# Optimization experiments

Hardware: AMD Instinct MI355X
Metric: run time of the kernel (lower is better)

Reference implementation:

```python
import jax, jax.numpy as jnp
import numpy as np

C = 16          # n_channels
HIDDEN = 128
ALPHA_THRESH = 0.1
STEP_SIZE = 1.0


def _perception_kernel():
    ident = jnp.array([[0., 0., 0.], [0., 1., 0.], [0., 0., 0.]], dtype=jnp.float32)
    dx = jnp.array([[-0.125, 0., 0.125], [-0.25, 0., 0.25], [-0.125, 0., 0.125]], dtype=jnp.float32)
    dy = dx.T  # angle = 0 -> no rotation
    k = jnp.stack([ident, dx, dy])                 # [3,3,3]
    return jnp.tile(k, (C, 1, 1))[:, None]          # [3C,1,3,3], OIHW, groups=C


def _wrap_pad(x):
    # circular padding of 1 on H and W (torus)
    return jnp.pad(x, ((0, 0), (0, 0), (1, 1), (1, 1)), mode='wrap')


def _living_mask(x):
    alpha = x[:, 3:4]                               # [B,1,H,W]
    pooled = jax.lax.reduce_window(_wrap_pad(alpha), -jnp.inf, jax.lax.max,
                                   (1, 1, 3, 3), (1, 1, 1, 1), 'VALID')
    return pooled > ALPHA_THRESH                    # [B,1,H,W] bool


def _perceive(x):
    kern = _perception_kernel()
    return jax.lax.conv_general_dilated(
        _wrap_pad(x), kern, window_strides=(1, 1), padding='VALID',
        feature_group_count=C,
        dimension_numbers=('NCHW', 'OIHW', 'NCHW'))   # [B,3C,H,W]


def setup_inputs() -> dict:
    key = jax.random.key(0)
    k1, k2, k3, k4 = jax.random.split(key, 4)
    B, H, W = 32, 256, 256
    x = jax.random.uniform(k1, (B, C, H, W), dtype=jnp.float32)
    fire_mask = jax.random.randint(k2, (B, 1, H, W), 0, 2).astype(jnp.int32)
    # Conv2d(48->128,1) and Conv2d(128->16,1) weights, stored as matrices
    w1 = jax.random.normal(k3, (HIDDEN, 3 * C), dtype=jnp.float32) * (1.0 / np.sqrt(3 * C))
    b1 = jnp.zeros((HIDDEN,), dtype=jnp.float32)
    w2 = jax.random.normal(k4, (C, HIDDEN), dtype=jnp.float32) * (1.0 / np.sqrt(HIDDEN))
    b2 = jnp.zeros((C,), dtype=jnp.float32)
    return {"x": x, "w1": w1, "b1": b1, "w2": w2, "b2": b2, "fire_mask": fire_mask}


def reference(x, w1, b1, w2, b2, fire_mask):
    pre_life = _living_mask(x)                                   # [B,1,H,W]
    y = _perceive(x)                                             # [B,3C,H,W]
    h = jax.nn.relu(jnp.einsum('bchw,oc->bohw', y, w1) + b1[None, :, None, None])
    dx = (jnp.einsum('bchw,oc->bohw', h, w2) + b2[None, :, None, None]) * STEP_SIZE
    dx = dx * fire_mask.astype(dx.dtype)                          # stochastic update mask
    x_new = x + dx
    post_life = _living_mask(x_new)
    life = (pre_life & post_life).astype(x_new.dtype)
    return x_new * life
```

## Files before the change

kernel.cpp:

```cpp
#include <hip/hip_runtime.h>
#include <hip/hip_bf16.h>


#define CCH 16
#define HID 128
#define HH 256
#define WW 256
#define BB 32

typedef __attribute__((ext_vector_type(8))) short bf16x8;
typedef __attribute__((ext_vector_type(4))) float f32x4;
typedef __attribute__((ext_vector_type(4))) int i32x4;
typedef __attribute__((ext_vector_type(2))) unsigned int u32x2;

union bfpack {
  u32x2 w2[2];
  bf16x8 v;
};

__device__ inline unsigned short f2bf(float f) {
  unsigned int u = __float_as_uint(f);
  u += 0x7FFFu + ((u >> 16) & 1u);
  return (unsigned short)(u >> 16);
}
__device__ inline float bf2f(unsigned short s) {
  return __uint_as_float(((unsigned int)s) << 16);
}
__device__ inline unsigned int cvtpk2(float a, float b) {
  union { __hip_bfloat162 h; unsigned int u; } cv;
  cv.h = __float22bfloat162_rn(make_float2(a, b));
  return cv.u;
}

__global__ __launch_bounds__(256) void pack_weights_kernel(
    const float* __restrict__ w1, const float* __restrict__ w2,
    unsigned short* __restrict__ w1p, unsigned short* __restrict__ w2p) {
  const int tid = blockIdx.x * 256 + threadIdx.x;
  if (tid < 2048) {
    const int l = tid & 63, m = (tid >> 6) & 7, ks = (tid >> 9) & 1,
              pl = (tid >> 10) & 1;
    const int row = m * 16 + (l & 15);
    const int kb = ks * 32 + (l >> 4) * 8;
    const size_t off = ((((size_t)pl * 2 + ks) * 8 + m) * 64 + l) * 8;
#pragma unroll
    for (int j = 0; j < 8; ++j) {
      const int k = kb + j;
      const int cc = k >> 2, f = k & 3;
      const float v = (f < 3) ? w1[row * 48 + cc * 3 + f] : 0.0f;
      const unsigned short hi = f2bf(v);
      w1p[off + j] = (pl == 0) ? hi : f2bf(v - bf2f(hi));
    }
  } else if (tid < 2560) {
    const int t2 = tid - 2048;
    const int l = t2 & 63, ks = (t2 >> 6) & 3, pl = (t2 >> 8) & 1;
    const int row = l & 15;
    const int kb = ks * 32 + (l >> 4) * 8;
    const size_t off = (((size_t)pl * 4 + ks) * 64 + l) * 8;
#pragma unroll
    for (int j = 0; j < 8; ++j) {
      const float v = w2[row * 128 + kb + j];
      const unsigned short hi = f2bf(v);
      w2p[off + j] = (pl == 0) ? hi : f2bf(v - bf2f(hi));
    }
  }
}

__device__ inline int swkey(int row) {
  return (((row >> 2) ^ ((row & 3) << 2)) & 15) << 3;
}

__global__ __launch_bounds__(256, 4) void nca_mfma_kernel(
    const float* __restrict__ x, const float* __restrict__ b1,
    const float* __restrict__ b2, const unsigned short* __restrict__ w1p,
    const unsigned short* __restrict__ w2p, const int* __restrict__ fire,
    float* __restrict__ out, float* __restrict__ alpha_ws,
    unsigned char* __restrict__ pre_ws) {
  __shared__ __align__(16) unsigned char smem[24576];
  unsigned char* Ys = smem;
  unsigned char* Hsm = smem + 8192;

  const int L = blockIdx.x;
  const int orig = ((L & 7) << 12) | (L >> 3);
  const int b = orig >> 10;
  const int h = (orig >> 2) & 255;
  const int wt = orig & 3;
  const int tid = threadIdx.x;
  const int wv = tid >> 6, lane = tid & 63, g = lane >> 4, ln = lane & 15;
  const int c = wv * 4 + g;
  const int q = ln;
  const int gcol0 = wt * 64 + q * 4;
  const int hm = (h + 255) & 255, hp = (h + 1) & 255;

  const float* xc = x + (size_t)(b * CCH + c) * (HH * WW);
  const f32x4 t4 = *(const f32x4*)(xc + (size_t)hm * WW + gcol0);
  const f32x4 m4 = *(const f32x4*)(xc + (size_t)h * WW + gcol0);
  const f32x4 o4 = *(const f32x4*)(xc + (size_t)hp * WW + gcol0);
  f32x4 av, bv;
#pragma unroll
  for (int j = 0; j < 4; ++j) {
    av[j] = 0.125f * (t4[j] + o4[j]) + 0.25f * m4[j];
    bv[j] = 0.125f * (o4[j] - t4[j]);
  }

  float haA = 0.f, haB = 0.f, hcm = 0.f;
  if (q == 0 || q == 15) {
    const int gc = (q == 15) ? ((wt * 64 + 64) & 255) : ((wt * 64 + 255) & 255);
    const float t = xc[(size_t)hm * WW + gc];
    const float m = xc[(size_t)h * WW + gc];
    const float bo = xc[(size_t)hp * WW + gc];
    haA = 0.125f * (t + bo) + 0.25f * m;
    haB = 0.125f * (bo - t);
    hcm = fmaxf(fmaxf(t, m), bo);
  }

  {
    float aLs = __shfl(av[3], lane - 1, 64);
    float bLs = __shfl(bv[3], lane - 1, 64);
    float aRs = __shfl(av[0], lane + 1, 64);
    float bRs = __shfl(bv[0], lane + 1, 64);
    if (q == 0) { aLs = haA; bLs = haB; }
    if (q == 15) { aRs = haA; bRs = haB; }

    const int c8 = c * 8;
#pragma unroll
    for (int i = 0; i < 4; ++i) {
      const float aR = (i < 3) ? av[i + 1] : aRs;
      const float aL = (i > 0) ? av[i - 1] : aLs;
      const float bR = (i < 3) ? bv[i + 1] : bRs;
      const float bL = (i > 0) ? bv[i - 1] : bLs;
      const float y0 = m4[i];
      const float y1 = aR - aL;
      const float y2 = bL + 2.0f * bv[i] + bR;
      const int px = q * 4 + i;
      u32x2 w;
      w[0] = cvtpk2(y0, y1);
      w[1] = cvtpk2(y2, 0.0f);
      *(u32x2*)(Ys + px * 128 + (c8 ^ swkey(px))) = w;
    }

    if (c == 3) {
      f32x4 cm4;
#pragma unroll
      for (int j = 0; j < 4; ++j) cm4[j] = fmaxf(fmaxf(t4[j], m4[j]), o4[j]);
      float cmL = __shfl(cm4[3], lane - 1, 64);
      float cmR = __shfl(cm4[0], lane + 1, 64);
      if (q == 0) cmL = hcm;
      if (q == 15) cmR = hcm;
      const float p0 = fmaxf(fmaxf(cmL, cm4[0]), cm4[1]);
      const float p1 = fmaxf(fmaxf(cm4[0], cm4[1]), cm4[2]);
      const float p2 = fmaxf(fmaxf(cm4[1], cm4[2]), cm4[3]);
      const float p3 = fmaxf(fmaxf(cm4[2], cm4[3]), cmR);
      const unsigned int pb = (p0 > 0.1f ? 1u : 0u) |
                              ((p1 > 0.1f ? 1u : 0u) << 8) |
                              ((p2 > 0.1f ? 1u : 0u) << 16) |
                              ((p3 > 0.1f ? 1u : 0u) << 24);
      const size_t pix0 = ((size_t)b * HH + h) * WW + gcol0;
      *(unsigned int*)(pre_ws + pix0) = pb;
    }
  }

  bf16x8 A1[2][4];
#pragma unroll
  for (int mi = 0; mi < 2; ++mi)
#pragma unroll
    for (int f = 0; f < 4; ++f)
      A1[mi][f] = *(const bf16x8*)(
          w1p + (((size_t)f * 8 + (wv * 2 + mi)) * 64 + lane) * 8);
  f32x4 b1v[2];
#pragma unroll
  for (int mi = 0; mi < 2; ++mi)
    b1v[mi] = *(const f32x4*)(b1 + (wv * 2 + mi) * 16 + g * 4);

  __syncthreads();

#pragma unroll
  for (int ni = 0; ni < 4; ++ni) {
    const int pxb = ni * 16 + ln;
    const int sk = swkey(pxb);
    const unsigned char* rb = Ys + pxb * 128;
    bfpack B0, B1;
    B0.w2[0] = *(const u32x2*)(rb + ((g * 16) ^ sk));
    B0.w2[1] = *(const u32x2*)(rb + ((g * 16 + 8) ^ sk));
    B1.w2[0] = *(const u32x2*)(rb + ((64 + g * 16) ^ sk));
    B1.w2[1] = *(const u32x2*)(rb + ((64 + g * 16 + 8) ^ sk));
#pragma unroll
    for (int mi = 0; mi < 2; ++mi) {
      f32x4 a = (f32x4){0.f, 0.f, 0.f, 0.f};
      a = __builtin_amdgcn_mfma_f32_16x16x32_bf16(A1[mi][0], B0.v, a, 0, 0, 0);
      a = __builtin_amdgcn_mfma_f32_16x16x32_bf16(A1[mi][1], B1.v, a, 0, 0, 0);
      a = __builtin_amdgcn_mfma_f32_16x16x32_bf16(A1[mi][2], B0.v, a, 0, 0, 0);
      a = __builtin_amdgcn_mfma_f32_16x16x32_bf16(A1[mi][3], B1.v, a, 0, 0, 0);
      const int hid0 = (wv * 2 + mi) * 16 + g * 4;
      u32x2 hv;
      hv[0] = cvtpk2(fmaxf(a[0] + b1v[mi][0], 0.f),
                     fmaxf(a[1] + b1v[mi][1], 0.f));
      hv[1] = cvtpk2(fmaxf(a[2] + b1v[mi][2], 0.f),
                     fmaxf(a[3] + b1v[mi][3], 0.f));
      *(u32x2*)(Hsm + pxb * 256 + ((hid0 * 2) ^ sk)) = hv;
    }
  }
  __syncthreads();

  {
    bf16x8 A2[8];
#pragma unroll
    for (int i = 0; i < 8; ++i)
      A2[i] = *(const bf16x8*)(w2p + ((size_t)i * 64 + lane) * 8);

    const int px0 = wv * 16 + g * 4;
    const int wg0 = wt * 64 + px0;
    const size_t pix0 = ((size_t)b * HH + h) * WW + wg0;
    const i32x4 fi = *(const i32x4*)(fire + pix0);
    const float b2v = b2[ln];
    const size_t xi0 = (((size_t)(b * CCH + ln)) * HH + h) * WW + wg0;
    const f32x4 xo = *(const f32x4*)(x + xi0);

    const int prow = wv * 16 + ln;
    const int sk = swkey(prow);
    const unsigned char* rb = Hsm + prow * 256;
    f32x4 a = (f32x4){0.f, 0.f, 0.f, 0.f};
#pragma unroll
    for (int ks = 0; ks < 4; ++ks) {
      const int o = ks * 64 + g * 16;
      bfpack Hf;
      Hf.w2[0] = *(const u32x2*)(rb + (o ^ sk));
      Hf.w2[1] = *(const u32x2*)(rb + ((o + 8) ^ sk));
      a = __builtin_amdgcn_mfma_f32_16x16x32_bf16(Hf.v, A2[ks], a, 0, 0, 0);
      a = __builtin_amdgcn_mfma_f32_16x16x32_bf16(Hf.v, A2[4 + ks], a, 0, 0, 0);
    }
    f32x4 v;
#pragma unroll
    for (int r = 0; r < 4; ++r) v[r] = xo[r] + (a[r] + b2v) * (float)fi[r];
    *(f32x4*)(out + xi0) = v;
    if (ln == 3) *(f32x4*)(alpha_ws + pix0) = v;
  }
}

__global__ __launch_bounds__(256) void life_mask_kernel(
    const float* __restrict__ alpha_ws, const unsigned char* __restrict__ pre_ws,
    float* __restrict__ out) {
  const int idx = blockIdx.x * 256 + threadIdx.x;
  const int lane = idx & 63;
  const int w0 = lane * 4;
  const int h = (idx >> 6) & 255;
  const int b = idx >> 14;
  const int hm = (h + 255) & 255;
  const int hp = (h + 1) & 255;

  const float* ab = alpha_ws + (size_t)b * HH * WW;
  const f32x4 up = *(const f32x4*)(ab + (size_t)hm * WW + w0);
  const f32x4 mi = *(const f32x4*)(ab + (size_t)h * WW + w0);
  const f32x4 dn = *(const f32x4*)(ab + (size_t)hp * WW + w0);
  f32x4 cm;
#pragma unroll
  for (int j = 0; j < 4; ++j) cm[j] = fmaxf(fmaxf(up[j], mi[j]), dn[j]);

  const float cmL = __shfl(cm[3], (lane + 63) & 63, 64);
  const float cmR = __shfl(cm[0], (lane + 1) & 63, 64);
  const float p0 = fmaxf(fmaxf(cmL, cm[0]), cm[1]);
  const float p1 = fmaxf(fmaxf(cm[0], cm[1]), cm[2]);
  const float p2 = fmaxf(fmaxf(cm[1], cm[2]), cm[3]);
  const float p3 = fmaxf(fmaxf(cm[2], cm[3]), cmR);

  const size_t pix0 = ((size_t)b * HH + h) * WW + w0;
  const unsigned int pb = *(const unsigned int*)(pre_ws + pix0);
  const bool l0 = (p0 > 0.1f) && (pb & 0xFFu);
  const bool l1 = (p1 > 0.1f) && (pb & 0xFF00u);
  const bool l2 = (p2 > 0.1f) && (pb & 0xFF0000u);
  const bool l3 = (p3 > 0.1f) && (pb & 0xFF000000u);

  if (!(l0 && l1 && l2 && l3)) {
    const bool lv[4] = {l0, l1, l2, l3};
#pragma unroll
    for (int r = 0; r < 4; ++r) {
      if (!lv[r]) {
        float* op = out + ((size_t)b * CCH * HH + h) * WW + w0 + r;
#pragma unroll
        for (int c = 0; c < CCH; ++c) op[(size_t)c * HH * WW] = 0.0f;
      }
    }
  }
}

extern "C" void kernel_launch(void* const* d_in, const int* in_sizes, int n_in,
                              void* d_out, int out_size, void* d_ws,
                              size_t ws_size, hipStream_t stream) {
  const float* x = (const float*)d_in[0];
  const float* w1 = (const float*)d_in[1];
  const float* b1 = (const float*)d_in[2];
  const float* w2 = (const float*)d_in[3];
  const float* b2 = (const float*)d_in[4];
  const int* fire = (const int*)d_in[5];
  float* out = (float*)d_out;

  const size_t npix = (size_t)BB * HH * WW;
  unsigned short* w1p = (unsigned short*)d_ws;
  unsigned short* w2p = (unsigned short*)((char*)d_ws + 32768);
  float* alpha_ws = (float*)((char*)d_ws + 40960);
  unsigned char* pre_ws = (unsigned char*)d_ws + 40960 + npix * sizeof(float);

  pack_weights_kernel<<<10, 256, 0, stream>>>(w1, w2, w1p, w2p);
  nca_mfma_kernel<<<BB * HH * 4, 256, 0, stream>>>(x, b1, b2, w1p, w2p, fire,
                                                   out, alpha_ws, pre_ws);
  life_mask_kernel<<<(int)(npix / 4 / 256), 256, 0, stream>>>(alpha_ws, pre_ws,
                                                              out);
}
```

Before: 172.7 us.

## Process full row per block with prefetched perception tiles and fold b1 into GEMM

Each block now handles a full 256-pixel row: four 64-column tiles instead of one. All four perception filters are computed up front, and three of them are held in registers. The block then cycles GEMM1, writes the next tile into LDS, and runs GEMM2. This is meant to overlap global loads with MFMA work and cut the block count by four. The first-layer bias is folded into the padding slot of the packed W1, with a constant 1 feeding that column, so the separate bias add disappears. The cost is more registers and more barriers per block, which could reduce occupancy.

```diff
diff --git a/kernel.cpp b/kernel.cpp
--- a/kernel.cpp
+++ b/kernel.cpp
@@ -33,8 +33,9 @@
 }
 
 __global__ __launch_bounds__(256) void pack_weights_kernel(
-    const float* __restrict__ w1, const float* __restrict__ w2,
-    unsigned short* __restrict__ w1p, unsigned short* __restrict__ w2p) {
+    const float* __restrict__ w1, const float* __restrict__ b1,
+    const float* __restrict__ w2, unsigned short* __restrict__ w1p,
+    unsigned short* __restrict__ w2p) {
   const int tid = blockIdx.x * 256 + threadIdx.x;
   if (tid < 2048) {
     const int l = tid & 63, m = (tid >> 6) & 7, ks = (tid >> 9) & 1,
@@ -46,7 +47,8 @@
     for (int j = 0; j < 8; ++j) {
       const int k = kb + j;
       const int cc = k >> 2, f = k & 3;
-      const float v = (f < 3) ? w1[row * 48 + cc * 3 + f] : 0.0f;
+      const float v = (f < 3) ? w1[row * 48 + cc * 3 + f]
+                              : ((k == 3) ? b1[row] : 0.0f);
       const unsigned short hi = f2bf(v);
       w1p[off + j] = (pl == 0) ? hi : f2bf(v - bf2f(hi));
     }
@@ -70,8 +72,8 @@
 }
 
 __global__ __launch_bounds__(256, 4) void nca_mfma_kernel(
-    const float* __restrict__ x, const float* __restrict__ b1,
-    const float* __restrict__ b2, const unsigned short* __restrict__ w1p,
+    const float* __restrict__ x, const float* __restrict__ b2,
+    const unsigned short* __restrict__ w1p,
     const unsigned short* __restrict__ w2p, const int* __restrict__ fire,
     float* __restrict__ out, float* __restrict__ alpha_ws,
     unsigned char* __restrict__ pre_ws) {
@@ -80,40 +82,42 @@
   unsigned char* Hsm = smem + 8192;
 
   const int L = blockIdx.x;
-  const int orig = ((L & 7) << 12) | (L >> 3);
-  const int b = orig >> 10;
-  const int h = (orig >> 2) & 255;
-  const int wt = orig & 3;
+  const int orig = ((L & 7) << 10) | (L >> 3);
+  const int b = orig >> 8;
+  const int h = orig & 255;
   const int tid = threadIdx.x;
   const int wv = tid >> 6, lane = tid & 63, g = lane >> 4, ln = lane & 15;
   const int c = wv * 4 + g;
   const int q = ln;
-  const int gcol0 = wt * 64 + q * 4;
   const int hm = (h + 255) & 255, hp = (h + 1) & 255;
-
   const float* xc = x + (size_t)(b * CCH + c) * (HH * WW);
-  const f32x4 t4 = *(const f32x4*)(xc + (size_t)hm * WW + gcol0);
-  const f32x4 m4 = *(const f32x4*)(xc + (size_t)h * WW + gcol0);
-  const f32x4 o4 = *(const f32x4*)(xc + (size_t)hp * WW + gcol0);
-  f32x4 av, bv;
-#pragma unroll
-  for (int j = 0; j < 4; ++j) {
-    av[j] = 0.125f * (t4[j] + o4[j]) + 0.25f * m4[j];
-    bv[j] = 0.125f * (o4[j] - t4[j]);
-  }
-
-  float haA = 0.f, haB = 0.f, hcm = 0.f;
-  if (q == 0 || q == 15) {
-    const int gc = (q == 15) ? ((wt * 64 + 64) & 255) : ((wt * 64 + 255) & 255);
-    const float t = xc[(size_t)hm * WW + gc];
-    const float m = xc[(size_t)h * WW + gc];
-    const float bo = xc[(size_t)hp * WW + gc];
-    haA = 0.125f * (t + bo) + 0.25f * m;
-    haB = 0.125f * (bo - t);
-    hcm = fmaxf(fmaxf(t, m), bo);
-  }
-
-  {
+  const float padv = (c == 0) ? 1.0f : 0.0f;
+  const bool edge = (q == 0 || q == 15);
+
+  u32x2 yP[3][4];
+
+  auto FILTER = [&](int wt_, u32x2* park) {
+    const int gcol0 = wt_ * 64 + q * 4;
+    const f32x4 t4 = *(const f32x4*)(xc + (size_t)hm * WW + gcol0);
+    const f32x4 m4 = *(const f32x4*)(xc + (size_t)h * WW + gcol0);
+    const f32x4 o4 = *(const f32x4*)(xc + (size_t)hp * WW + gcol0);
+    f32x4 av, bv;
+#pragma unroll
+    for (int j = 0; j < 4; ++j) {
+      av[j] = 0.125f * (t4[j] + o4[j]) + 0.25f * m4[j];
+      bv[j] = 0.125f * (o4[j] - t4[j]);
+    }
+    float haA = 0.f, haB = 0.f, hcm = 0.f;
+    if (edge) {
+      const int gc =
+          (q == 15) ? ((wt_ * 64 + 64) & 255) : ((wt_ * 64 + 255) & 255);
+      const float t = xc[(size_t)hm * WW + gc];
+      const float m = xc[(size_t)h * WW + gc];
+      const float bo = xc[(size_t)hp * WW + gc];
+      haA = 0.125f * (t + bo) + 0.25f * m;
+      haB = 0.125f * (bo - t);
+      hcm = fmaxf(fmaxf(t, m), bo);
+    }
     float aLs = __shfl(av[3], lane - 1, 64);
     float bLs = __shfl(bv[3], lane - 1, 64);
     float aRs = __shfl(av[0], lane + 1, 64);
@@ -128,16 +132,13 @@
       const float aL = (i > 0) ? av[i - 1] : aLs;
       const float bR = (i < 3) ? bv[i + 1] : bRs;
       const float bL = (i > 0) ? bv[i - 1] : bLs;
-      const float y0 = m4[i];
-      const float y1 = aR - aL;
-      const float y2 = bL + 2.0f * bv[i] + bR;
       const int px = q * 4 + i;
       u32x2 w;
-      w[0] = cvtpk2(y0, y1);
-      w[1] = cvtpk2(y2, 0.0f);
-      *(u32x2*)(Ys + px * 128 + (c8 ^ swkey(px))) = w;
-    }
-
+      w[0] = cvtpk2(m4[i], aR - aL);
+      w[1] = cvtpk2(bL + 2.0f * bv[i] + bR, padv);
+      if (park) park[i] = w;
+      else *(u32x2*)(Ys + px * 128 + (c8 ^ swkey(px))) = w;
+    }
     if (c == 3) {
       f32x4 cm4;
 #pragma unroll
@@ -154,10 +155,14 @@
                               ((p1 > 0.1f ? 1u : 0u) << 8) |
                               ((p2 > 0.1f ? 1u : 0u) << 16) |
                               ((p3 > 0.1f ? 1u : 0u) << 24);
-      const size_t pix0 = ((size_t)b * HH + h) * WW + gcol0;
-      *(unsigned int*)(pre_ws + pix0) = pb;
-    }
-  }
+      *(unsigned int*)(pre_ws + ((size_t)b * HH + h) * WW + gcol0) = pb;
+    }
+  };
+
+  FILTER(0, nullptr);
+  FILTER(1, yP[0]);
+  FILTER(2, yP[1]);
+  FILTER(3, yP[2]);
 
   bf16x8 A1[2][4];
 #pragma unroll
@@ -166,49 +171,42 @@
     for (int f = 0; f < 4; ++f)
       A1[mi][f] = *(const bf16x8*)(
           w1p + (((size_t)f * 8 + (wv * 2 + mi)) * 64 + lane) * 8);
-  f32x4 b1v[2];
-#pragma unroll
-  for (int mi = 0; mi < 2; ++mi)
-    b1v[mi] = *(const f32x4*)(b1 + (wv * 2 + mi) * 16 + g * 4);
-
-  __syncthreads();
-
-#pragma unroll
-  for (int ni = 0; ni < 4; ++ni) {
-    const int pxb = ni * 16 + ln;
-    const int sk = swkey(pxb);
-    const unsigned char* rb = Ys + pxb * 128;
-    bfpack B0, B1;
-    B0.w2[0] = *(const u32x2*)(rb + ((g * 16) ^ sk));
-    B0.w2[1] = *(const u32x2*)(rb + ((g * 16 + 8) ^ sk));
-    B1.w2[0] = *(const u32x2*)(rb + ((64 + g * 16) ^ sk));
-    B1.w2[1] = *(const u32x2*)(rb + ((64 + g * 16 + 8) ^ sk));
-#pragma unroll
-    for (int mi = 0; mi < 2; ++mi) {
-      f32x4 a = (f32x4){0.f, 0.f, 0.f, 0.f};
-      a = __builtin_amdgcn_mfma_f32_16x16x32_bf16(A1[mi][0], B0.v, a, 0, 0, 0);
-      a = __builtin_amdgcn_mfma_f32_16x16x32_bf16(A1[mi][1], B1.v, a, 0, 0, 0);
-      a = __builtin_amdgcn_mfma_f32_16x16x32_bf16(A1[mi][2], B0.v, a, 0, 0, 0);
-      a = __builtin_amdgcn_mfma_f32_16x16x32_bf16(A1[mi][3], B1.v, a, 0, 0, 0);
-      const int hid0 = (wv * 2 + mi) * 16 + g * 4;
-      u32x2 hv;
-      hv[0] = cvtpk2(fmaxf(a[0] + b1v[mi][0], 0.f),
-                     fmaxf(a[1] + b1v[mi][1], 0.f));
-      hv[1] = cvtpk2(fmaxf(a[2] + b1v[mi][2], 0.f),
-                     fmaxf(a[3] + b1v[mi][3], 0.f));
-      *(u32x2*)(Hsm + pxb * 256 + ((hid0 * 2) ^ sk)) = hv;
-    }
-  }
-  __syncthreads();
-
-  {
+
+  auto GEMM1 = [&]() {
+#pragma unroll
+    for (int ni = 0; ni < 4; ++ni) {
+      const int pxb = ni * 16 + ln;
+      const int sk = swkey(pxb);
+      const unsigned char* rb = Ys + pxb * 128;
+      bfpack B0, B1;
+      B0.w2[0] = *(const u32x2*)(rb + ((g * 16) ^ sk));
+      B0.w2[1] = *(const u32x2*)(rb + ((g * 16 + 8) ^ sk));
+      B1.w2[0] = *(const u32x2*)(rb + ((64 + g * 16) ^ sk));
+      B1.w2[1] = *(const u32x2*)(rb + ((64 + g * 16 + 8) ^ sk));
+#pragma unroll
+      for (int mi = 0; mi < 2; ++mi) {
+        f32x4 a = (f32x4){0.f, 0.f, 0.f, 0.f};
+        a = __builtin_amdgcn_mfma_f32_16x16x32_bf16(A1[mi][0], B0.v, a, 0, 0, 0);
+        a = __builtin_amdgcn_mfma_f32_16x16x32_bf16(A1[mi][1], B1.v, a, 0, 0, 0);
+        a = __builtin_amdgcn_mfma_f32_16x16x32_bf16(A1[mi][2], B0.v, a, 0, 0, 0);
+        a = __builtin_amdgcn_mfma_f32_16x16x32_bf16(A1[mi][3], B1.v, a, 0, 0, 0);
+        const int hid0 = (wv * 2 + mi) * 16 + g * 4;
+        u32x2 hv;
+        hv[0] = cvtpk2(fmaxf(a[0], 0.f), fmaxf(a[1], 0.f));
+        hv[1] = cvtpk2(fmaxf(a[2], 0.f), fmaxf(a[3], 0.f));
+        *(u32x2*)(Hsm + pxb * 256 + ((hid0 * 2) ^ sk)) = hv;
+      }
+    }
+  };
+
+  auto GEMM2 = [&](int wt_) {
     bf16x8 A2[8];
 #pragma unroll
     for (int i = 0; i < 8; ++i)
       A2[i] = *(const bf16x8*)(w2p + ((size_t)i * 64 + lane) * 8);
 
     const int px0 = wv * 16 + g * 4;
-    const int wg0 = wt * 64 + px0;
+    const int wg0 = wt_ * 64 + px0;
     const size_t pix0 = ((size_t)b * HH + h) * WW + wg0;
     const i32x4 fi = *(const i32x4*)(fire + pix0);
     const float b2v = b2[ln];
@@ -233,7 +231,36 @@
     for (int r = 0; r < 4; ++r) v[r] = xo[r] + (a[r] + b2v) * (float)fi[r];
     *(f32x4*)(out + xi0) = v;
     if (ln == 3) *(f32x4*)(alpha_ws + pix0) = v;
-  }
+  };
+
+  auto PARK = [&](const u32x2* yp) {
+    const int c8 = c * 8;
+#pragma unroll
+    for (int i = 0; i < 4; ++i) {
+      const int px = q * 4 + i;
+      *(u32x2*)(Ys + px * 128 + (c8 ^ swkey(px))) = yp[i];
+    }
+  };
+
+  __syncthreads();
+  GEMM1();
+  __syncthreads();
+  PARK(yP[0]);
+  GEMM2(0);
+  __syncthreads();
+  GEMM1();
+  __syncthreads();
+  PARK(yP[1]);
+  GEMM2(1);
+  __syncthreads();
+  GEMM1();
+  __syncthreads();
+  PARK(yP[2]);
+  GEMM2(2);
+  __syncthreads();
+  GEMM1();
+  __syncthreads();
+  GEMM2(3);
 }
 
 __global__ __launch_bounds__(256) void life_mask_kernel(
@@ -299,9 +326,9 @@
   float* alpha_ws = (float*)((char*)d_ws + 40960);
   unsigned char* pre_ws = (unsigned char*)d_ws + 40960 + npix * sizeof(float);
 
-  pack_weights_kernel<<<10, 256, 0, stream>>>(w1, w2, w1p, w2p);
-  nca_mfma_kernel<<<BB * HH * 4, 256, 0, stream>>>(x, b1, b2, w1p, w2p, fire,
-                                                   out, alpha_ws, pre_ws);
+  pack_weights_kernel<<<10, 256, 0, stream>>>(w1, b1, w2, w1p, w2p);
+  nca_mfma_kernel<<<BB * HH, 256, 0, stream>>>(x, b2, w1p, w2p, fire, out,
+                                               alpha_ws, pre_ws);
   life_mask_kernel<<<(int)(npix / 4 / 256), 256, 0, stream>>>(alpha_ws, pre_ws,
                                                               out);
 }
```

Result: slower. 408.9 us (+136.7%).
